# Performance work log

Hardware: AMD Instinct MI355X
Metric: run time of the kernel (lower is better)

## Reference

```python
import math
import jax, jax.numpy as jnp
import numpy as np

B, L, D, H = 8, 512, 768, 12
DK = D // H  # 64


def setup_inputs() -> dict:
    key = jax.random.key(0)
    ks = jax.random.split(key, 8)
    x = jax.random.normal(ks[0], (B, L, D), dtype=jnp.float32)
    mask = jnp.zeros((B, L), dtype=jnp.float32)            # 0 = valid, -10000 = pad (torch convention here)
    roots_label = jax.random.randint(ks[1], (B, L), 0, 2, dtype=jnp.int32)
    root_mask = jnp.ones((B, L), dtype=jnp.int32)          # only checked for not-None in the original
    W_SCALE = 0.02  # keep exp(scores) well-conditioned, as trained weights would
    Wq = jax.random.normal(ks[2], (D, D), dtype=jnp.float32) * W_SCALE
    bq = jnp.zeros((D,), dtype=jnp.float32)
    Wk = jax.random.normal(ks[3], (D, D), dtype=jnp.float32) * W_SCALE
    bk = jnp.zeros((D,), dtype=jnp.float32)
    Wr = jax.random.normal(ks[4], (D, 1), dtype=jnp.float32) * W_SCALE
    br = jnp.zeros((1,), dtype=jnp.float32)
    return {"x": x, "mask": mask, "roots_label": roots_label, "root_mask": root_mask,
            "Wq": Wq, "bq": bq, "Wk": Wk, "bk": bk, "Wr": Wr, "br": br}


def _matrix_tree_multi(scores, root):
    # scores: [B,H,L,L], root: [B,L,1]  (multi-head branch of _getMatrixTree_multi)
    A = jnp.exp(scores)                                   # [B,H,L,L]
    R = jnp.broadcast_to(jnp.exp(root)[..., 0][:, None, :], A.shape[:3])  # [B,H,L]
    col_sum = jnp.sum(A, axis=2)                          # [B,H,L]  (torch.sum(A, 2))
    eye = jnp.eye(A.shape[-1], dtype=A.dtype)
    # LL = diag(col_sum) - A + diag(R)
    LL = (col_sum + R)[..., :, None] * eye - A * (1.0 - eye) - A * eye + A * eye  # keep exact: diag(col_sum+R) - A
    LL = (col_sum + R)[..., :, None] * eye - A
    LL_inv = jnp.linalg.inv(LL)                           # [B,H,L,L]
    LL_inv_diag = jnp.diagonal(LL_inv, axis1=-2, axis2=-1)  # [B,H,L]
    d0 = R * LL_inv_diag                                  # root marginals [B,H,L]
    tmp1 = A * LL_inv_diag[..., None, :]                  # = transpose(A^T * diag[...,:,None])
    tmp2 = A * jnp.swapaxes(LL_inv, -2, -1)
    d = tmp1 - tmp2                                       # edge marginals [B,H,L,L]
    return d, d0


def reference(x, mask, roots_label, root_mask, Wq, bq, Wk, bk, Wr, br):
    key = x @ Wk + bk                                     # [B,L,D]
    query = (x @ Wq + bq) / math.sqrt(D)
    root = x @ Wr + br                                    # [B,L,1]
    q = query.reshape(B, L, H, DK).transpose(0, 2, 1, 3)  # [B,H,L,DK]
    k = key.reshape(B, L, H, DK).transpose(0, 2, 1, 3)
    scores = jnp.einsum('bhqd,bhkd->bhqk', q, k)          # [B,H,L,L]
    m = mask / -10000.0                                   # 1 at padded positions
    root = jnp.clip(root - m[:, :, None] * 50.0, -40.0, None)
    sm = jnp.broadcast_to(m[:, None, :, None], (B, H, L, L))  # scores_mask
    scores = jnp.clip(scores - sm * 50.0 - jnp.swapaxes(sm, -2, -1) * 50.0, -40.0, None)
    d, d0 = _matrix_tree_multi(scores, root)
    # root BCE loss summed over heads, masked-mean with labels
    labels = roots_label.reshape(-1).astype(jnp.float32)  # [B*L]
    p = jnp.clip(d0.astype(jnp.float32), 1e-5, 1.0 - 1e-5)
    p_h = jnp.moveaxis(p, 1, 0).reshape(H, -1)            # [H, B*L]
    bce = -(labels * jnp.log(p_h) + (1.0 - labels) * jnp.log(1.0 - p_h))
    loss_root = (bce.sum(axis=0) * labels).mean()
    attn = jnp.swapaxes(d, -2, -1)
    sm_sym = (sm + jnp.swapaxes(sm, -2, -1)).astype(bool)
    attn = jnp.where(sm_sym, 0.0, attn)
    context = jnp.einsum('bhqk,bkd->bhqd', attn, x)       # [B,H,L,D]
    return context, d, d0, loss_root
```

## Files before the change

kernel.cpp:

```cpp
#include <hip/hip_runtime.h>
#include <hip/hip_bf16.h>
#include <math.h>


#define INV_SQRT_D 0.03608439182435161f

typedef short bf16x8 __attribute__((ext_vector_type(8)));
typedef float f32x4 __attribute__((ext_vector_type(4)));
typedef unsigned int u32x4 __attribute__((ext_vector_type(4)));

__device__ __forceinline__ void mm_micro(const float* At, const float* Bt,
                                         float acc[8][8], int tx, int ty)
{
#pragma unroll
  for (int t = 0; t < 16; ++t) {
    const float4 a0 = *(const float4*)(At + t*132 + ty*8);
    const float4 a1 = *(const float4*)(At + t*132 + ty*8 + 4);
    const float4 b0 = *(const float4*)(Bt + t*132 + tx*8);
    const float4 b1 = *(const float4*)(Bt + t*132 + tx*8 + 4);
    const float a[8] = {a0.x,a0.y,a0.z,a0.w,a1.x,a1.y,a1.z,a1.w};
    const float b[8] = {b0.x,b0.y,b0.z,b0.w,b1.x,b1.y,b1.z,b1.w};
#pragma unroll
    for (int i = 0; i < 8; ++i)
#pragma unroll
      for (int j = 0; j < 8; ++j)
        acc[i][j] = fmaf(a[i], b[j], acc[i][j]);
  }
}

__global__ __launch_bounds__(256) void proj_kernel(
    const float* __restrict__ x,
    const float* __restrict__ Wq, const float* __restrict__ bq,
    const float* __restrict__ Wk, const float* __restrict__ bk,
    float* __restrict__ Q, float* __restrict__ Kc)
{
  const float* W; const float* bias; float* out; float scale;
  if (blockIdx.z == 0) { W = Wq; bias = bq; out = Q;  scale = INV_SQRT_D; }
  else                 { W = Wk; bias = bk; out = Kc; scale = 1.0f; }

  __shared__ __align__(16) float At[16*132];
  __shared__ __align__(16) float Bt[16*132];

  const int tx = threadIdx.x, ty = threadIdx.y;
  const int tid = ty*16 + tx;
  const int row0 = blockIdx.y * 128, col0 = blockIdx.x * 128;
  const int lt = tid & 15, lr = tid >> 4;
  const int bc = tid & 127, btr = tid >> 7;

  float acc[8][8] = {};

  for (int kk = 0; kk < 768; kk += 16) {
#pragma unroll
    for (int u = 0; u < 8; ++u) {
      const int r = lr + 16*u;
      At[lt*132 + r] = x[(size_t)(row0 + r)*768 + kk + lt];
    }
#pragma unroll
    for (int u = 0; u < 8; ++u) {
      const int t = btr + 2*u;
      Bt[t*132 + bc] = W[(size_t)(kk + t)*768 + col0 + bc];
    }
    __syncthreads();
    mm_micro(At, Bt, acc, tx, ty);
    __syncthreads();
  }

#pragma unroll
  for (int i = 0; i < 8; ++i) {
    const int r = row0 + ty*8 + i;
#pragma unroll
    for (int j = 0; j < 8; j += 4) {
      const int c = col0 + tx*8 + j;
      float4 v;
      v.x = (acc[i][j+0] + bias[c+0]) * scale;
      v.y = (acc[i][j+1] + bias[c+1]) * scale;
      v.z = (acc[i][j+2] + bias[c+2]) * scale;
      v.w = (acc[i][j+3] + bias[c+3]) * scale;
      *(float4*)(out + (size_t)r*768 + c) = v;
    }
  }
}

__global__ __launch_bounds__(256) void root_kernel(
    const float* __restrict__ x, const float* __restrict__ Wr,
    const float* __restrict__ br, const float* __restrict__ mask,
    float* __restrict__ Rv, float* __restrict__ mv)
{
  const int n = blockIdx.x*4 + (threadIdx.x >> 6);
  const int lane = threadIdx.x & 63;
  float s = 0.0f;
  for (int c = lane; c < 768; c += 64) s += x[(size_t)n*768 + c] * Wr[c];
#pragma unroll
  for (int off = 32; off > 0; off >>= 1) s += __shfl_down(s, off, 64);
  if (lane == 0) {
    const float root = s + br[0];
    const float m = mask[n] * (-1e-4f);
    Rv[n] = expf(fmaxf(root - m*50.0f, -40.0f));
    mv[n] = m;
  }
}

__global__ __launch_bounds__(256) void scores_kernel(
    const float* __restrict__ Qs, const float* __restrict__ Ks,
    const float* __restrict__ mv, float* __restrict__ A)
{
  const int bh = blockIdx.z, b = bh / 12, h = bh % 12;
  const int i0 = blockIdx.y * 128, j0 = blockIdx.x * 128;
  __shared__ __align__(16) float At[16*132];
  __shared__ __align__(16) float Bt[16*132];
  const int tx = threadIdx.x, ty = threadIdx.y;
  const int tid = ty*16 + tx;
  const int lt = tid & 15, lr = tid >> 4;
  const size_t qbase = (size_t)(b*512 + i0)*768 + h*64;
  const size_t kbase = (size_t)(b*512 + j0)*768 + h*64;

  float acc[8][8] = {};

  for (int kk = 0; kk < 64; kk += 16) {
#pragma unroll
    for (int u = 0; u < 8; ++u) {
      const int r = lr + 16*u;
      At[lt*132 + r] = Qs[qbase + (size_t)r*768 + kk + lt];
      Bt[lt*132 + r] = Ks[kbase + (size_t)r*768 + kk + lt];
    }
    __syncthreads();
    mm_micro(At, Bt, acc, tx, ty);
    __syncthreads();
  }

  float mi[8], mj[8];
#pragma unroll
  for (int i = 0; i < 8; ++i) mi[i] = mv[b*512 + i0 + ty*8 + i];
#pragma unroll
  for (int j = 0; j < 8; ++j) mj[j] = mv[b*512 + j0 + tx*8 + j];

#pragma unroll
  for (int i = 0; i < 8; ++i) {
    const size_t rowb = (size_t)(bh*512 + i0 + ty*8 + i)*512;
#pragma unroll
    for (int j = 0; j < 8; j += 4) {
      float4 v;
      v.x = expf(fmaxf(acc[i][j+0] - (mi[i]+mj[j+0])*50.0f, -40.0f));
      v.y = expf(fmaxf(acc[i][j+1] - (mi[i]+mj[j+1])*50.0f, -40.0f));
      v.z = expf(fmaxf(acc[i][j+2] - (mi[i]+mj[j+2])*50.0f, -40.0f));
      v.w = expf(fmaxf(acc[i][j+3] - (mi[i]+mj[j+3])*50.0f, -40.0f));
      *(float4*)(A + rowb + j0 + tx*8 + j) = v;
    }
  }
}

__global__ __launch_bounds__(256) void pack_x_kernel(
    const float* __restrict__ x, unsigned int* __restrict__ xh,
    unsigned int* __restrict__ xl)
{
  const int gid = blockIdx.x*256 + threadIdx.x;
  const int k2g = gid / 192;
  const int cc  = (gid - k2g*192) * 4;
  const unsigned int* xb = (const unsigned int*)x;
  const size_t s0 = (size_t)(2*k2g)*768 + cc;
  const uint4 r0 = *(const uint4*)(xb + s0);
  const uint4 r1 = *(const uint4*)(xb + s0 + 768);
  unsigned int hw[4], lw[4];
#pragma unroll
  for (int i = 0; i < 4; ++i) {
    const unsigned int u0 = ((const unsigned int*)&r0)[i];
    const unsigned int u1 = ((const unsigned int*)&r1)[i];
    const unsigned int h0 = (u0 + 0x7FFFu + ((u0 >> 16) & 1u)) >> 16;
    const unsigned int h1 = (u1 + 0x7FFFu + ((u1 >> 16) & 1u)) >> 16;
    hw[i] = h0 | (h1 << 16);
    const float rs0 = __uint_as_float(u0) - __uint_as_float(h0 << 16);
    const float rs1 = __uint_as_float(u1) - __uint_as_float(h1 << 16);
    lw[i] = __builtin_amdgcn_perm(__float_as_uint(rs1), __float_as_uint(rs0),
                                  0x07060302u);
  }
  const size_t o = (size_t)k2g*768 + cc;
  *(uint4*)(xh + o) = make_uint4(hw[0], hw[1], hw[2], hw[3]);
  *(uint4*)(xl + o) = make_uint4(lw[0], lw[1], lw[2], lw[3]);
}

__global__ void colsum_kernel(const float* __restrict__ A, float* __restrict__ colsum)
{
  const int bh = blockIdx.y;
  const int j = blockIdx.x*256 + threadIdx.x;
  const float* Ab = A + (size_t)bh*262144;
  float s = 0.0f;
  for (int i = 0; i < 512; ++i) s += Ab[(size_t)i*512 + j];
  colsum[bh*512 + j] = s;
}

__global__ void buildM_kernel(const float* __restrict__ A, const float* __restrict__ colsum,
                              const float* __restrict__ Rv, float* __restrict__ M)
{
  const size_t g = ((size_t)blockIdx.x*256 + threadIdx.x)*4;
  const int bh = (int)(g >> 18);
  const int i = (int)((g >> 9) & 511);
  const int j = (int)(g & 511);
  const float4 a = *(const float4*)(A + g);
  float4 v; v.x = -a.x; v.y = -a.y; v.z = -a.z; v.w = -a.w;
  if (i >= j && i < j+4) {
    const float dadd = colsum[bh*512 + i] + Rv[(bh/12)*512 + i];
    ((float*)&v)[i - j] += dadd;
  }
  *(float4*)(M + g) = v;
}

__global__ __launch_bounds__(256) void gj_inv_kernel(
    const float* __restrict__ M, float* __restrict__ Mp,
    float* __restrict__ Inv, int k0)
{
  const float* const Mg  = M   + (size_t)blockIdx.x * 262144;
  float* const Mpg       = Mp  + (size_t)blockIdx.x * 32768;
  float* const Ig        = Inv + (size_t)blockIdx.x * 4096;
  const int tid = threadIdx.x;

  if (tid >= 64) {
    const int t = tid - 64;
    for (int p = 0; p < 43; ++p) {
      const int idx = p*192 + t;
      if (idx < 8192) {
        const int r = idx >> 7, c = (idx & 127) * 4;
        *(float4*)(Mpg + (size_t)r*512 + c) =
            *(const float4*)(Mg + (size_t)(k0 + r)*512 + c);
      }
    }
    return;
  }

  const int lane = tid;
  float w[64];
  {
    const float* src = Mg + (size_t)(k0 + lane)*512 + k0;
#pragma unroll
    for (int q = 0; q < 16; ++q) {
      const float4 t4 = *(const float4*)(src + q*4);
      w[q*4+0]=t4.x; w[q*4+1]=t4.y; w[q*4+2]=t4.z; w[q*4+3]=t4.w;
    }
  }

  float fcur = w[0];
#pragma unroll 1
  for (int kk = 0; kk < 64; ++kk) {
    float rj[64];
#pragma unroll
    for (int j = 0; j < 64; ++j) rj[j] = __shfl(w[j], kk);
    const float pv = __shfl(fcur, kk);
    const float p  = 1.0f / pv;
    const bool isp = (lane == kk);
    const float alpha = isp ? p : -fcur * p;
    float fnext = fcur;
#pragma unroll
    for (int j = 0; j < 64; ++j) {
      const float base = isp ? 0.0f : w[j];
      float val = fmaf(alpha, rj[j], base);
      if (j == kk) val = alpha;
      w[j] = val;
      if (j == kk + 1) fnext = val;
    }
    fcur = fnext;
  }

  {
    float* dst = Ig + lane*64;
#pragma unroll
    for (int q = 0; q < 16; ++q)
      *(float4*)(dst + q*4) = make_float4(w[q*4+0], w[q*4+1], w[q*4+2], w[q*4+3]);
  }
}

__global__ __launch_bounds__(256) void gj_w_kernel(
    float* __restrict__ M, const float* __restrict__ Inv, int k0)
{
  const int bh = blockIdx.y;
  const int row0 = blockIdx.x * 128;
  float* const Mg = M + (size_t)bh*262144;
  const float* const Ig = Inv + (size_t)bh*4096;

  __shared__ __align__(16) float Ct[16*132];
  __shared__ __align__(16) float It[16*68];

  const int tx = threadIdx.x, ty = threadIdx.y;
  const int tid = ty*16 + tx;
  const int lt = tid & 15, lr = tid >> 4;

  float acc[8][4] = {};

  for (int kc = 0; kc < 64; kc += 16) {
#pragma unroll
    for (int u = 0; u < 8; ++u) {
      const int r = lr + 16*u;
      Ct[lt*132 + r] = Mg[(size_t)(row0 + r)*512 + k0 + kc + lt];
    }
    {
      const int j = tid & 63, t0 = tid >> 6;
#pragma unroll
      for (int u = 0; u < 4; ++u) {
        const int t = t0*4 + u;
        It[t*68 + j] = Ig[(kc + t)*64 + j];
      }
    }
    __syncthreads();
#pragma unroll
    for (int t = 0; t < 16; ++t) {
      const float4 a0 = *(const float4*)(Ct + t*132 + ty*8);
      const float4 a1 = *(const float4*)(Ct + t*132 + ty*8 + 4);
      const float4 b  = *(const float4*)(It + t*68 + tx*4);
      const float a[8] = {a0.x,a0.y,a0.z,a0.w,a1.x,a1.y,a1.z,a1.w};
      const float bb[4] = {b.x,b.y,b.z,b.w};
#pragma unroll
      for (int i = 0; i < 8; ++i)
#pragma unroll
        for (int j = 0; j < 4; ++j)
          acc[i][j] = fmaf(a[i], bb[j], acc[i][j]);
    }
    __syncthreads();
  }

#pragma unroll
  for (int i = 0; i < 8; ++i) {
    const int irow = row0 + ty*8 + i;
    float4 v;
    if (irow >= k0 && irow < k0 + 64) {
      v = *(const float4*)(Ig + (irow - k0)*64 + tx*4);
    } else {
      v = make_float4(-acc[i][0], -acc[i][1], -acc[i][2], -acc[i][3]);
    }
    *(float4*)(Mg + (size_t)irow*512 + k0 + tx*4) = v;
  }
}

__global__ __launch_bounds__(256) void gj_update_kernel(
    float* __restrict__ M, const float* __restrict__ Mp, int k0)
{
  const int bh = blockIdx.z;
  const int row0 = blockIdx.y * 128, col0 = blockIdx.x * 128;
  float* const Mg = M + (size_t)bh*262144;
  const float* const Mpg = Mp + (size_t)bh*32768;

  __shared__ __align__(16) float At[16*132];
  __shared__ __align__(16) float Bt[16*132];
  const int tx = threadIdx.x, ty = threadIdx.y;
  const int tid = ty*16 + tx;
  const int lt = tid & 15, lr = tid >> 4;
  const int bc = tid & 127, btr = tid >> 7;

  float acc[8][8] = {};

  for (int kc = 0; kc < 64; kc += 16) {
#pragma unroll
    for (int u = 0; u < 8; ++u) {
      const int r = lr + 16*u;
      At[lt*132 + r] = Mg[(size_t)(row0 + r)*512 + k0 + kc + lt];
    }
#pragma unroll
    for (int u = 0; u < 8; ++u) {
      const int t = btr + 2*u;
      Bt[t*132 + bc] = Mpg[(size_t)(kc + t)*512 + col0 + bc];
    }
    __syncthreads();
    mm_micro(At, Bt, acc, tx, ty);
    __syncthreads();
  }

#pragma unroll
  for (int ii = 0; ii < 8; ++ii) {
    const int irow = row0 + ty*8 + ii;
    const bool inP = (irow >= k0) && (irow < k0 + 64);
#pragma unroll
    for (int jj = 0; jj < 8; jj += 4) {
      const int jcol = col0 + tx*8 + jj;
      if (jcol >= k0 && jcol < k0 + 64) continue;
      float* cell = Mg + (size_t)irow*512 + jcol;
      float4 v = make_float4(acc[ii][jj+0], acc[ii][jj+1], acc[ii][jj+2], acc[ii][jj+3]);
      if (!inP) {
        const float4 o = *(const float4*)cell;
        v.x += o.x; v.y += o.y; v.z += o.z; v.w += o.w;
      }
      *(float4*)cell = v;
    }
  }
}

__global__ void diag_d0_kernel(const float* __restrict__ Minv, const float* __restrict__ Rv,
                               float* __restrict__ diagv, float* __restrict__ d0)
{
  const int bh = blockIdx.x, l = threadIdx.x;
  const float dg = Minv[(size_t)bh*262144 + (size_t)l*513];
  diagv[bh*512 + l] = dg;
  d0[bh*512 + l] = Rv[(bh/12)*512 + l] * dg;
}

__global__ __launch_bounds__(1024) void loss_kernel(const float* __restrict__ d0,
                                                    const int* __restrict__ labels,
                                                    float* __restrict__ loss)
{
  float acc = 0.0f;
  for (int n = threadIdx.x; n < 4096; n += 1024) {
    if (labels[n] != 0) {
      const int b = n >> 9, l = n & 511;
      float s = 0.0f;
#pragma unroll
      for (int h = 0; h < 12; ++h) {
        float p = d0[(size_t)(b*12 + h)*512 + l];
        p = fminf(fmaxf(p, 1e-5f), 1.0f - 1e-5f);
        s -= logf(p);
      }
      acc += s;
    }
  }
  __shared__ float red[16];
#pragma unroll
  for (int off = 32; off > 0; off >>= 1) acc += __shfl_down(acc, off, 64);
  const int wv = threadIdx.x >> 6, ln = threadIdx.x & 63;
  if (ln == 0) red[wv] = acc;
  __syncthreads();
  if (threadIdx.x == 0) {
    float t = 0.0f;
    for (int w2 = 0; w2 < 16; ++w2) t += red[w2];
    loss[0] = t * (1.0f/4096.0f);
  }
}

__global__ __launch_bounds__(256) void finalize_d_kernel(
    float* __restrict__ dmat, const float* __restrict__ Minv, const float* __restrict__ diagv)
{
  const int bh = blockIdx.z;
  const int i0 = blockIdx.y*64, j0 = blockIdx.x*64;
  __shared__ float t[64][65];
  const int tx = threadIdx.x, ty = threadIdx.y;
  const size_t mbase = (size_t)bh*262144;
  for (int jj = ty; jj < 64; jj += 4)
    t[jj][tx] = Minv[mbase + (size_t)(j0+jj)*512 + i0 + tx];
  __syncthreads();
  const float dg_j = diagv[bh*512 + j0 + tx];
  for (int ii = ty; ii < 64; ii += 4) {
    const size_t idx = mbase + (size_t)(i0+ii)*512 + j0 + tx;
    dmat[idx] = dmat[idx] * (dg_j - t[tx][ii]);
  }
}

__global__ __launch_bounds__(256) void context_packed_kernel(
    const float* __restrict__ dmat, const unsigned int* __restrict__ xh,
    const unsigned int* __restrict__ xl, const float* __restrict__ mv,
    float* __restrict__ ctx)
{
  const int bh = blockIdx.z + 8, b = bh / 12;
  const int q0 = blockIdx.y << 7;
  const int c0 = blockIdx.x << 7;

  __shared__ __align__(16) unsigned int AhL[16*132];
  __shared__ __align__(16) unsigned int AlL[16*132];
  __shared__ __align__(16) unsigned int BhL[16*132];
  __shared__ __align__(16) unsigned int BlL[16*132];

  const int tid = threadIdx.x;
  const int w = tid >> 6, l = tid & 63;
  const int wq = w >> 1, wc = w & 1;
  const int l15 = l & 15, g = l >> 4;
  const int q4 = tid & 31, pp = tid >> 5;

  const size_t dbase = (size_t)bh*262144;
  const int xrow0 = b*256;

  float mq[4];
  {
    const float4 t4 = *(const float4*)(mv + b*512 + q0 + q4*4);
    mq[0]=t4.x; mq[1]=t4.y; mq[2]=t4.z; mq[3]=t4.w;
  }

  f32x4 acc[4][4] = {};

  for (int kk = 0; kk < 512; kk += 32) {
    __syncthreads();
#pragma unroll
    for (int s = 0; s < 2; ++s) {
      const int k2 = pp + 8*s;
      const int krow = kk + 2*k2;
      const float mk0 = mv[b*512 + krow];
      const float mk1 = mv[b*512 + krow + 1];
      const uint4 r0 = *(const uint4*)(dmat + dbase + (size_t)krow*512 + q0 + q4*4);
      const uint4 r1 = *(const uint4*)(dmat + dbase + (size_t)(krow+1)*512 + q0 + q4*4);
      unsigned int hw[4], lw[4];
#pragma unroll
      for (int i = 0; i < 4; ++i) {
        unsigned int v0 = ((const unsigned int*)&r0)[i];
        unsigned int v1 = ((const unsigned int*)&r1)[i];
        v0 = ((mk0 + mq[i]) != 0.0f) ? 0u : v0;
        v1 = ((mk1 + mq[i]) != 0.0f) ? 0u : v1;
        hw[i] = __builtin_amdgcn_perm(v1, v0, 0x07060302u);
        const float f0 = __uint_as_float(v0) - __uint_as_float(v0 & 0xffff0000u);
        const float f1 = __uint_as_float(v1) - __uint_as_float(v1 & 0xffff0000u);
        lw[i] = __builtin_amdgcn_perm(__float_as_uint(f1), __float_as_uint(f0),
                                      0x07060302u);
      }
      *(uint4*)(AhL + k2*132 + q4*4) = make_uint4(hw[0], hw[1], hw[2], hw[3]);
      *(uint4*)(AlL + k2*132 + q4*4) = make_uint4(lw[0], lw[1], lw[2], lw[3]);
      const size_t xi = (size_t)(xrow0 + (kk >> 1) + k2)*768 + c0 + q4*4;
      *(uint4*)(BhL + k2*132 + q4*4) = *(const uint4*)(xh + xi);
      *(uint4*)(BlL + k2*132 + q4*4) = *(const uint4*)(xl + xi);
    }
    __syncthreads();

    u32x4 ah[4], al[4], bhv[4], blv[4];
#pragma unroll
    for (int mi = 0; mi < 4; ++mi) {
      const int col = wq*64 + mi*16 + l15;
#pragma unroll
      for (int d2 = 0; d2 < 4; ++d2) {
        ah[mi][d2] = AhL[(4*g + d2)*132 + col];
        al[mi][d2] = AlL[(4*g + d2)*132 + col];
      }
    }
#pragma unroll
    for (int ni = 0; ni < 4; ++ni) {
      const int col = wc*64 + ni*16 + l15;
#pragma unroll
      for (int d2 = 0; d2 < 4; ++d2) {
        bhv[ni][d2] = BhL[(4*g + d2)*132 + col];
        blv[ni][d2] = BlL[(4*g + d2)*132 + col];
      }
    }

#pragma unroll
    for (int mi = 0; mi < 4; ++mi) {
      const bf16x8 Ah = __builtin_bit_cast(bf16x8, ah[mi]);
      const bf16x8 Al = __builtin_bit_cast(bf16x8, al[mi]);
#pragma unroll
      for (int ni = 0; ni < 4; ++ni) {
        const bf16x8 Bh = __builtin_bit_cast(bf16x8, bhv[ni]);
        const bf16x8 Bl = __builtin_bit_cast(bf16x8, blv[ni]);
        acc[mi][ni] = __builtin_amdgcn_mfma_f32_16x16x32_bf16(Ah, Bh, acc[mi][ni], 0, 0, 0);
        acc[mi][ni] = __builtin_amdgcn_mfma_f32_16x16x32_bf16(Ah, Bl, acc[mi][ni], 0, 0, 0);
        acc[mi][ni] = __builtin_amdgcn_mfma_f32_16x16x32_bf16(Al, Bh, acc[mi][ni], 0, 0, 0);
      }
    }
  }

#pragma unroll
  for (int mi = 0; mi < 4; ++mi) {
    const int row = q0 + wq*64 + mi*16 + g*4;
#pragma unroll
    for (int ni = 0; ni < 4; ++ni) {
      const int col = c0 + wc*64 + ni*16 + l15;
#pragma unroll
      for (int r = 0; r < 4; ++r)
        ctx[((size_t)bh*512 + row + r)*768 + col] = acc[mi][ni][r];
    }
  }
}

__device__ __forceinline__ unsigned int pack_bf16x2(float v)
{
  const unsigned int u = __float_as_uint(v);
  const unsigned int hi = (u + 0x7FFFu + ((u >> 16) & 1u)) >> 16;
  const float hf = __uint_as_float(hi << 16);
  const unsigned int lo = __float_as_uint(v - hf) >> 16;
  return hi | (lo << 16);
}

__global__ __launch_bounds__(256) void context_mfma_kernel(
    const float* __restrict__ dmat, const float* __restrict__ x,
    const float* __restrict__ mv, float* __restrict__ ctx)
{
  const int bh = blockIdx.z, b = bh / 12;
  const int q0 = blockIdx.y << 7;
  const int c0 = blockIdx.x << 7;

  __shared__ unsigned int As[32*133];
  __shared__ unsigned int Bs[32*133];

  const int tid = threadIdx.x;
  const int w = tid >> 6, l = tid & 63;
  const int wq = w >> 1, wc = w & 1;
  const int l15 = l & 15, g = l >> 4;
  const int q4 = tid & 31, kr0 = tid >> 5;

  const size_t dbase = (size_t)bh*262144;
  const size_t xbase = (size_t)b*393216;

  float mq[4];
  {
    const float4 t4 = *(const float4*)(mv + b*512 + q0 + q4*4);
    mq[0]=t4.x; mq[1]=t4.y; mq[2]=t4.z; mq[3]=t4.w;
  }

  f32x4 acc[4][4] = {};

  for (int kk = 0; kk < 512; kk += 32) {
    __syncthreads();
#pragma unroll
    for (int p = 0; p < 4; ++p) {
      const int kr = kr0 + 8*p;
      const int krow = kk + kr;
      const float mk = mv[b*512 + krow];
      const float4 av = *(const float4*)(dmat + dbase + (size_t)krow*512 + q0 + q4*4);
      const float4 bv = *(const float4*)(x + xbase + (size_t)krow*768 + c0 + q4*4);
      unsigned int* aw = As + kr*133 + q4*4;
      unsigned int* bw = Bs + kr*133 + q4*4;
      aw[0] = pack_bf16x2(((mk + mq[0]) != 0.0f) ? 0.0f : av.x);
      aw[1] = pack_bf16x2(((mk + mq[1]) != 0.0f) ? 0.0f : av.y);
      aw[2] = pack_bf16x2(((mk + mq[2]) != 0.0f) ? 0.0f : av.z);
      aw[3] = pack_bf16x2(((mk + mq[3]) != 0.0f) ? 0.0f : av.w);
      bw[0] = pack_bf16x2(bv.x);
      bw[1] = pack_bf16x2(bv.y);
      bw[2] = pack_bf16x2(bv.z);
      bw[3] = pack_bf16x2(bv.w);
    }
    __syncthreads();

    u32x4 ah[4], al[4], bhv[4], blv[4];
#pragma unroll
    for (int mi = 0; mi < 4; ++mi) {
      const unsigned int* base = As + g*8*133 + (wq*64 + mi*16 + l15);
      unsigned int u[8];
#pragma unroll
      for (int e = 0; e < 8; ++e) u[e] = base[e*133];
#pragma unroll
      for (int d2 = 0; d2 < 4; ++d2) {
        ah[mi][d2] = __builtin_amdgcn_perm(u[2*d2+1], u[2*d2], 0x05040100u);
        al[mi][d2] = __builtin_amdgcn_perm(u[2*d2+1], u[2*d2], 0x07060302u);
      }
    }
#pragma unroll
    for (int ni = 0; ni < 4; ++ni) {
      const unsigned int* base = Bs + g*8*133 + (wc*64 + ni*16 + l15);
      unsigned int u[8];
#pragma unroll
      for (int e = 0; e < 8; ++e) u[e] = base[e*133];
#pragma unroll
      for (int d2 = 0; d2 < 4; ++d2) {
        bhv[ni][d2] = __builtin_amdgcn_perm(u[2*d2+1], u[2*d2], 0x05040100u);
        blv[ni][d2] = __builtin_amdgcn_perm(u[2*d2+1], u[2*d2], 0x07060302u);
      }
    }

#pragma unroll
    for (int mi = 0; mi < 4; ++mi) {
      const bf16x8 Ah = __builtin_bit_cast(bf16x8, ah[mi]);
      const bf16x8 Al = __builtin_bit_cast(bf16x8, al[mi]);
#pragma unroll
      for (int ni = 0; ni < 4; ++ni) {
        const bf16x8 Bh = __builtin_bit_cast(bf16x8, bhv[ni]);
        const bf16x8 Bl = __builtin_bit_cast(bf16x8, blv[ni]);
        acc[mi][ni] = __builtin_amdgcn_mfma_f32_16x16x32_bf16(Ah, Bh, acc[mi][ni], 0, 0, 0);
        acc[mi][ni] = __builtin_amdgcn_mfma_f32_16x16x32_bf16(Ah, Bl, acc[mi][ni], 0, 0, 0);
        acc[mi][ni] = __builtin_amdgcn_mfma_f32_16x16x32_bf16(Al, Bh, acc[mi][ni], 0, 0, 0);
      }
    }
  }

#pragma unroll
  for (int mi = 0; mi < 4; ++mi) {
    const int row = q0 + wq*64 + mi*16 + g*4;
#pragma unroll
    for (int ni = 0; ni < 4; ++ni) {
      const int col = c0 + wc*64 + ni*16 + l15;
#pragma unroll
      for (int r = 0; r < 4; ++r)
        ctx[((size_t)bh*512 + row + r)*768 + col] = acc[mi][ni][r];
    }
  }
}

extern "C" void kernel_launch(void* const* d_in, const int* in_sizes, int n_in,
                              void* d_out, int out_size, void* d_ws, size_t ws_size,
                              hipStream_t stream)
{
  (void)in_sizes; (void)n_in; (void)out_size; (void)ws_size;

  const float* x    = (const float*)d_in[0];
  const float* mask = (const float*)d_in[1];
  const int*   roots= (const int*)d_in[2];
  const float* Wq   = (const float*)d_in[4];
  const float* bq   = (const float*)d_in[5];
  const float* Wk   = (const float*)d_in[6];
  const float* bk   = (const float*)d_in[7];
  const float* Wr   = (const float*)d_in[8];
  const float* br   = (const float*)d_in[9];

  float* out        = (float*)d_out;
  float* ctx_region = out;
  float* d_region   = out + 37748736;
  float* d0_region  = out + 62914560;
  float* loss_ptr   = out + 62963712;

  float* Qs = ctx_region;
  float* Ks = ctx_region + 3145728;
  float* Mv = ctx_region + 6291456;
  float* Mp = ctx_region + 31457280;
  float* Invs = ctx_region + 34603008;

  unsigned int* xh = (unsigned int*)ctx_region;
  unsigned int* xl = (unsigned int*)ctx_region + 1572864;

  float* ws     = (float*)d_ws;
  float* Rv     = ws;
  float* mv     = ws + 4096;
  float* colsum = ws + 8192;
  float* diagv  = ws + 57344;

  proj_kernel   <<<dim3(6,32,2),  dim3(16,16), 0, stream>>>(x, Wq, bq, Wk, bk, Qs, Ks);
  root_kernel   <<<dim3(1024),    dim3(256),   0, stream>>>(x, Wr, br, mask, Rv, mv);
  scores_kernel <<<dim3(4,4,96),  dim3(16,16), 0, stream>>>(Qs, Ks, mv, d_region);
  pack_x_kernel <<<dim3(1536),    dim3(256),   0, stream>>>(x, xh, xl);
  colsum_kernel <<<dim3(2,96),    dim3(256),   0, stream>>>(d_region, colsum);
  buildM_kernel <<<dim3(24576),   dim3(256),   0, stream>>>(d_region, colsum, Rv, Mv);

  for (int step = 0; step < 8; ++step) {
    const int k0 = step * 64;
    gj_inv_kernel   <<<dim3(96),     dim3(256),   0, stream>>>(Mv, Mp, Invs, k0);
    gj_w_kernel     <<<dim3(4,96),   dim3(16,16), 0, stream>>>(Mv, Invs, k0);
    gj_update_kernel<<<dim3(4,4,96), dim3(16,16), 0, stream>>>(Mv, Mp, k0);
  }

  diag_d0_kernel<<<dim3(96),      dim3(512),   0, stream>>>(Mv, Rv, diagv, d0_region);
  loss_kernel   <<<dim3(1),       dim3(1024),  0, stream>>>(d0_region, roots, loss_ptr);
  finalize_d_kernel<<<dim3(8,8,96), dim3(64,4), 0, stream>>>(d_region, Mv, diagv);
  context_packed_kernel<<<dim3(6,4,88), dim3(256), 0, stream>>>(d_region, xh, xl, mv, ctx_region);
  context_mfma_kernel  <<<dim3(6,4,8),  dim3(256), 0, stream>>>(d_region, x, mv, ctx_region);
}
```

Measured before the change: 1.909 ms.

## Use split-bf16 MFMA for Q/K projection and move panel copy into gj_w

Replaces the FP32 SIMT projection GEMM with a bf16 MFMA kernel using a three-term hi/lo split to keep near-FP32 accuracy, with weights pre-split by a new pack kernel. Also moves the pivot-row panel copy out of the single-block-per-head inversion kernel into the wider gj_w kernel, shrinking gj_inv to one wave. This removes FP32 FMA cost in the projection and the serial panel copy from each elimination step. The cost is an extra packing pass, more workspace, and a possible race if panel rows are modified before other blocks copy them.

```diff
diff --git a/kernel.cpp b/kernel.cpp
--- a/kernel.cpp
+++ b/kernel.cpp
@@ -28,138 +28,23 @@
   }
 }
 
-__global__ __launch_bounds__(256) void proj_kernel(
-    const float* __restrict__ x,
-    const float* __restrict__ Wq, const float* __restrict__ bq,
-    const float* __restrict__ Wk, const float* __restrict__ bk,
-    float* __restrict__ Q, float* __restrict__ Kc)
-{
-  const float* W; const float* bias; float* out; float scale;
-  if (blockIdx.z == 0) { W = Wq; bias = bq; out = Q;  scale = INV_SQRT_D; }
-  else                 { W = Wk; bias = bk; out = Kc; scale = 1.0f; }
-
-  __shared__ __align__(16) float At[16*132];
-  __shared__ __align__(16) float Bt[16*132];
-
-  const int tx = threadIdx.x, ty = threadIdx.y;
-  const int tid = ty*16 + tx;
-  const int row0 = blockIdx.y * 128, col0 = blockIdx.x * 128;
-  const int lt = tid & 15, lr = tid >> 4;
-  const int bc = tid & 127, btr = tid >> 7;
-
-  float acc[8][8] = {};
-
-  for (int kk = 0; kk < 768; kk += 16) {
-#pragma unroll
-    for (int u = 0; u < 8; ++u) {
-      const int r = lr + 16*u;
-      At[lt*132 + r] = x[(size_t)(row0 + r)*768 + kk + lt];
-    }
-#pragma unroll
-    for (int u = 0; u < 8; ++u) {
-      const int t = btr + 2*u;
-      Bt[t*132 + bc] = W[(size_t)(kk + t)*768 + col0 + bc];
-    }
-    __syncthreads();
-    mm_micro(At, Bt, acc, tx, ty);
-    __syncthreads();
-  }
-
-#pragma unroll
-  for (int i = 0; i < 8; ++i) {
-    const int r = row0 + ty*8 + i;
-#pragma unroll
-    for (int j = 0; j < 8; j += 4) {
-      const int c = col0 + tx*8 + j;
-      float4 v;
-      v.x = (acc[i][j+0] + bias[c+0]) * scale;
-      v.y = (acc[i][j+1] + bias[c+1]) * scale;
-      v.z = (acc[i][j+2] + bias[c+2]) * scale;
-      v.w = (acc[i][j+3] + bias[c+3]) * scale;
-      *(float4*)(out + (size_t)r*768 + c) = v;
-    }
-  }
-}
-
-__global__ __launch_bounds__(256) void root_kernel(
-    const float* __restrict__ x, const float* __restrict__ Wr,
-    const float* __restrict__ br, const float* __restrict__ mask,
-    float* __restrict__ Rv, float* __restrict__ mv)
-{
-  const int n = blockIdx.x*4 + (threadIdx.x >> 6);
-  const int lane = threadIdx.x & 63;
-  float s = 0.0f;
-  for (int c = lane; c < 768; c += 64) s += x[(size_t)n*768 + c] * Wr[c];
-#pragma unroll
-  for (int off = 32; off > 0; off >>= 1) s += __shfl_down(s, off, 64);
-  if (lane == 0) {
-    const float root = s + br[0];
-    const float m = mask[n] * (-1e-4f);
-    Rv[n] = expf(fmaxf(root - m*50.0f, -40.0f));
-    mv[n] = m;
-  }
-}
-
-__global__ __launch_bounds__(256) void scores_kernel(
-    const float* __restrict__ Qs, const float* __restrict__ Ks,
-    const float* __restrict__ mv, float* __restrict__ A)
-{
-  const int bh = blockIdx.z, b = bh / 12, h = bh % 12;
-  const int i0 = blockIdx.y * 128, j0 = blockIdx.x * 128;
-  __shared__ __align__(16) float At[16*132];
-  __shared__ __align__(16) float Bt[16*132];
-  const int tx = threadIdx.x, ty = threadIdx.y;
-  const int tid = ty*16 + tx;
-  const int lt = tid & 15, lr = tid >> 4;
-  const size_t qbase = (size_t)(b*512 + i0)*768 + h*64;
-  const size_t kbase = (size_t)(b*512 + j0)*768 + h*64;
-
-  float acc[8][8] = {};
-
-  for (int kk = 0; kk < 64; kk += 16) {
-#pragma unroll
-    for (int u = 0; u < 8; ++u) {
-      const int r = lr + 16*u;
-      At[lt*132 + r] = Qs[qbase + (size_t)r*768 + kk + lt];
-      Bt[lt*132 + r] = Ks[kbase + (size_t)r*768 + kk + lt];
-    }
-    __syncthreads();
-    mm_micro(At, Bt, acc, tx, ty);
-    __syncthreads();
-  }
-
-  float mi[8], mj[8];
-#pragma unroll
-  for (int i = 0; i < 8; ++i) mi[i] = mv[b*512 + i0 + ty*8 + i];
-#pragma unroll
-  for (int j = 0; j < 8; ++j) mj[j] = mv[b*512 + j0 + tx*8 + j];
-
-#pragma unroll
-  for (int i = 0; i < 8; ++i) {
-    const size_t rowb = (size_t)(bh*512 + i0 + ty*8 + i)*512;
-#pragma unroll
-    for (int j = 0; j < 8; j += 4) {
-      float4 v;
-      v.x = expf(fmaxf(acc[i][j+0] - (mi[i]+mj[j+0])*50.0f, -40.0f));
-      v.y = expf(fmaxf(acc[i][j+1] - (mi[i]+mj[j+1])*50.0f, -40.0f));
-      v.z = expf(fmaxf(acc[i][j+2] - (mi[i]+mj[j+2])*50.0f, -40.0f));
-      v.w = expf(fmaxf(acc[i][j+3] - (mi[i]+mj[j+3])*50.0f, -40.0f));
-      *(float4*)(A + rowb + j0 + tx*8 + j) = v;
-    }
-  }
-}
-
-__global__ __launch_bounds__(256) void pack_x_kernel(
-    const float* __restrict__ x, unsigned int* __restrict__ xh,
-    unsigned int* __restrict__ xl)
+__global__ __launch_bounds__(256) void pack_w_kernel(
+    const float* __restrict__ Wq, const float* __restrict__ Wk,
+    unsigned int* __restrict__ Wqh, unsigned int* __restrict__ Wql,
+    unsigned int* __restrict__ Wkh, unsigned int* __restrict__ Wkl)
 {
   const int gid = blockIdx.x*256 + threadIdx.x;
-  const int k2g = gid / 192;
-  const int cc  = (gid - k2g*192) * 4;
-  const unsigned int* xb = (const unsigned int*)x;
-  const size_t s0 = (size_t)(2*k2g)*768 + cc;
-  const uint4 r0 = *(const uint4*)(xb + s0);
-  const uint4 r1 = *(const uint4*)(xb + s0 + 768);
+  const int m = gid >= 73728;
+  const int id = m ? gid - 73728 : gid;
+  const int k2 = id / 192;
+  const int cc = (id - k2*192) * 4;
+  const float* W = m ? Wk : Wq;
+  unsigned int* Oh = m ? Wkh : Wqh;
+  unsigned int* Ol = m ? Wkl : Wql;
+  const unsigned int* wb = (const unsigned int*)W;
+  const size_t s0 = (size_t)(2*k2)*768 + cc;
+  const uint4 r0 = *(const uint4*)(wb + s0);
+  const uint4 r1 = *(const uint4*)(wb + s0 + 768);
   unsigned int hw[4], lw[4];
 #pragma unroll
   for (int i = 0; i < 4; ++i) {
@@ -173,6 +58,214 @@
     lw[i] = __builtin_amdgcn_perm(__float_as_uint(rs1), __float_as_uint(rs0),
                                   0x07060302u);
   }
+  const size_t o = (size_t)k2*768 + cc;
+  *(uint4*)(Oh + o) = make_uint4(hw[0], hw[1], hw[2], hw[3]);
+  *(uint4*)(Ol + o) = make_uint4(lw[0], lw[1], lw[2], lw[3]);
+}
+
+__global__ __launch_bounds__(256) void proj_mfma_kernel(
+    const float* __restrict__ x,
+    const unsigned int* __restrict__ Wqh, const unsigned int* __restrict__ Wql,
+    const unsigned int* __restrict__ Wkh, const unsigned int* __restrict__ Wkl,
+    const float* __restrict__ bq, const float* __restrict__ bk,
+    float* __restrict__ Q, float* __restrict__ Kc)
+{
+  const unsigned int* Wh; const unsigned int* Wl;
+  const float* bias; float* out; float scale;
+  if (blockIdx.z == 0) { Wh = Wqh; Wl = Wql; bias = bq; out = Q;  scale = INV_SQRT_D; }
+  else                 { Wh = Wkh; Wl = Wkl; bias = bk; out = Kc; scale = 1.0f; }
+
+  const int row0 = blockIdx.y << 7;
+  const int col0 = blockIdx.x << 7;
+
+  __shared__ __align__(16) unsigned int AhL[16*132];
+  __shared__ __align__(16) unsigned int AlL[16*132];
+  __shared__ __align__(16) unsigned int BhL[16*132];
+  __shared__ __align__(16) unsigned int BlL[16*132];
+
+  const int tid = threadIdx.x;
+  const int w = tid >> 6, l = tid & 63;
+  const int wq = w >> 1, wc = w & 1;
+  const int l15 = l & 15, g = l >> 4;
+  const int q4 = tid & 31, pp = tid >> 5;
+  const int an = tid & 127, ahh = tid >> 7;
+
+  f32x4 acc[4][4] = {};
+
+  for (int kk = 0; kk < 768; kk += 32) {
+    __syncthreads();
+#pragma unroll
+    for (int s = 0; s < 2; ++s) {
+      const int k2 = pp + 8*s;
+      const size_t wi = (size_t)((kk >> 1) + k2)*768 + col0 + q4*4;
+      *(uint4*)(BhL + k2*132 + q4*4) = *(const uint4*)(Wh + wi);
+      *(uint4*)(BlL + k2*132 + q4*4) = *(const uint4*)(Wl + wi);
+    }
+    {
+      const float* xr = x + (size_t)(row0 + an)*768 + kk + ahh*16;
+      const uint4 v0 = *(const uint4*)(xr + 0);
+      const uint4 v1 = *(const uint4*)(xr + 4);
+      const uint4 v2 = *(const uint4*)(xr + 8);
+      const uint4 v3 = *(const uint4*)(xr + 12);
+      const unsigned int uu[16] = {v0.x,v0.y,v0.z,v0.w, v1.x,v1.y,v1.z,v1.w,
+                                   v2.x,v2.y,v2.z,v2.w, v3.x,v3.y,v3.z,v3.w};
+#pragma unroll
+      for (int pr = 0; pr < 8; ++pr) {
+        const unsigned int a0 = uu[2*pr], a1 = uu[2*pr+1];
+        const unsigned int hw = __builtin_amdgcn_perm(a1, a0, 0x07060302u);
+        const float f0 = __uint_as_float(a0) - __uint_as_float(a0 & 0xffff0000u);
+        const float f1 = __uint_as_float(a1) - __uint_as_float(a1 & 0xffff0000u);
+        const unsigned int lw = __builtin_amdgcn_perm(__float_as_uint(f1),
+                                                      __float_as_uint(f0),
+                                                      0x07060302u);
+        const int k2 = ahh*8 + pr;
+        AhL[k2*132 + an] = hw;
+        AlL[k2*132 + an] = lw;
+      }
+    }
+    __syncthreads();
+
+    u32x4 ah[4], al[4], bhv[4], blv[4];
+#pragma unroll
+    for (int mi = 0; mi < 4; ++mi) {
+      const int col = wq*64 + mi*16 + l15;
+#pragma unroll
+      for (int d2 = 0; d2 < 4; ++d2) {
+        ah[mi][d2] = AhL[(4*g + d2)*132 + col];
+        al[mi][d2] = AlL[(4*g + d2)*132 + col];
+      }
+    }
+#pragma unroll
+    for (int ni = 0; ni < 4; ++ni) {
+      const int col = wc*64 + ni*16 + l15;
+#pragma unroll
+      for (int d2 = 0; d2 < 4; ++d2) {
+        bhv[ni][d2] = BhL[(4*g + d2)*132 + col];
+        blv[ni][d2] = BlL[(4*g + d2)*132 + col];
+      }
+    }
+
+#pragma unroll
+    for (int mi = 0; mi < 4; ++mi) {
+      const bf16x8 Ah = __builtin_bit_cast(bf16x8, ah[mi]);
+      const bf16x8 Al = __builtin_bit_cast(bf16x8, al[mi]);
+#pragma unroll
+      for (int ni = 0; ni < 4; ++ni) {
+        const bf16x8 Bh = __builtin_bit_cast(bf16x8, bhv[ni]);
+        const bf16x8 Bl = __builtin_bit_cast(bf16x8, blv[ni]);
+        acc[mi][ni] = __builtin_amdgcn_mfma_f32_16x16x32_bf16(Ah, Bh, acc[mi][ni], 0, 0, 0);
+        acc[mi][ni] = __builtin_amdgcn_mfma_f32_16x16x32_bf16(Ah, Bl, acc[mi][ni], 0, 0, 0);
+        acc[mi][ni] = __builtin_amdgcn_mfma_f32_16x16x32_bf16(Al, Bh, acc[mi][ni], 0, 0, 0);
+      }
+    }
+  }
+
+#pragma unroll
+  for (int mi = 0; mi < 4; ++mi) {
+    const int row = row0 + wq*64 + mi*16 + g*4;
+#pragma unroll
+    for (int ni = 0; ni < 4; ++ni) {
+      const int col = col0 + wc*64 + ni*16 + l15;
+      const float bs = bias[col];
+#pragma unroll
+      for (int r = 0; r < 4; ++r)
+        out[(size_t)(row + r)*768 + col] = (acc[mi][ni][r] + bs) * scale;
+    }
+  }
+}
+
+__global__ __launch_bounds__(256) void root_kernel(
+    const float* __restrict__ x, const float* __restrict__ Wr,
+    const float* __restrict__ br, const float* __restrict__ mask,
+    float* __restrict__ Rv, float* __restrict__ mv)
+{
+  const int n = blockIdx.x*4 + (threadIdx.x >> 6);
+  const int lane = threadIdx.x & 63;
+  float s = 0.0f;
+  for (int c = lane; c < 768; c += 64) s += x[(size_t)n*768 + c] * Wr[c];
+#pragma unroll
+  for (int off = 32; off > 0; off >>= 1) s += __shfl_down(s, off, 64);
+  if (lane == 0) {
+    const float root = s + br[0];
+    const float m = mask[n] * (-1e-4f);
+    Rv[n] = expf(fmaxf(root - m*50.0f, -40.0f));
+    mv[n] = m;
+  }
+}
+
+__global__ __launch_bounds__(256) void scores_kernel(
+    const float* __restrict__ Qs, const float* __restrict__ Ks,
+    const float* __restrict__ mv, float* __restrict__ A)
+{
+  const int bh = blockIdx.z, b = bh / 12, h = bh % 12;
+  const int i0 = blockIdx.y * 128, j0 = blockIdx.x * 128;
+  __shared__ __align__(16) float At[16*132];
+  __shared__ __align__(16) float Bt[16*132];
+  const int tx = threadIdx.x, ty = threadIdx.y;
+  const int tid = ty*16 + tx;
+  const int lt = tid & 15, lr = tid >> 4;
+  const size_t qbase = (size_t)(b*512 + i0)*768 + h*64;
+  const size_t kbase = (size_t)(b*512 + j0)*768 + h*64;
+
+  float acc[8][8] = {};
+
+  for (int kk = 0; kk < 64; kk += 16) {
+#pragma unroll
+    for (int u = 0; u < 8; ++u) {
+      const int r = lr + 16*u;
+      At[lt*132 + r] = Qs[qbase + (size_t)r*768 + kk + lt];
+      Bt[lt*132 + r] = Ks[kbase + (size_t)r*768 + kk + lt];
+    }
+    __syncthreads();
+    mm_micro(At, Bt, acc, tx, ty);
+    __syncthreads();
+  }
+
+  float mi[8], mj[8];
+#pragma unroll
+  for (int i = 0; i < 8; ++i) mi[i] = mv[b*512 + i0 + ty*8 + i];
+#pragma unroll
+  for (int j = 0; j < 8; ++j) mj[j] = mv[b*512 + j0 + tx*8 + j];
+
+#pragma unroll
+  for (int i = 0; i < 8; ++i) {
+    const size_t rowb = (size_t)(bh*512 + i0 + ty*8 + i)*512;
+#pragma unroll
+    for (int j = 0; j < 8; j += 4) {
+      float4 v;
+      v.x = expf(fmaxf(acc[i][j+0] - (mi[i]+mj[j+0])*50.0f, -40.0f));
+      v.y = expf(fmaxf(acc[i][j+1] - (mi[i]+mj[j+1])*50.0f, -40.0f));
+      v.z = expf(fmaxf(acc[i][j+2] - (mi[i]+mj[j+2])*50.0f, -40.0f));
+      v.w = expf(fmaxf(acc[i][j+3] - (mi[i]+mj[j+3])*50.0f, -40.0f));
+      *(float4*)(A + rowb + j0 + tx*8 + j) = v;
+    }
+  }
+}
+
+__global__ __launch_bounds__(256) void pack_x_kernel(
+    const float* __restrict__ x, unsigned int* __restrict__ xh,
+    unsigned int* __restrict__ xl)
+{
+  const int gid = blockIdx.x*256 + threadIdx.x;
+  const int k2g = gid / 192;
+  const int cc  = (gid - k2g*192) * 4;
+  const unsigned int* xb = (const unsigned int*)x;
+  const size_t s0 = (size_t)(2*k2g)*768 + cc;
+  const uint4 r0 = *(const uint4*)(xb + s0);
+  const uint4 r1 = *(const uint4*)(xb + s0 + 768);
+  unsigned int hw[4], lw[4];
+#pragma unroll
+  for (int i = 0; i < 4; ++i) {
+    const unsigned int u0 = ((const unsigned int*)&r0)[i];
+    const unsigned int u1 = ((const unsigned int*)&r1)[i];
+    const unsigned int h0 = (u0 + 0x7FFFu + ((u0 >> 16) & 1u)) >> 16;
+    const unsigned int h1 = (u1 + 0x7FFFu + ((u1 >> 16) & 1u)) >> 16;
+    hw[i] = h0 | (h1 << 16);
+    const float rs0 = __uint_as_float(u0) - __uint_as_float(h0 << 16);
+    const float rs1 = __uint_as_float(u1) - __uint_as_float(h1 << 16);
+    lw[i] = __builtin_amdgcn_perm(__float_as_uint(rs1), __float_as_uint(rs0),
+                                  0x07060302u);
+  }
   const size_t o = (size_t)k2g*768 + cc;
   *(uint4*)(xh + o) = make_uint4(hw[0], hw[1], hw[2], hw[3]);
   *(uint4*)(xl + o) = make_uint4(lw[0], lw[1], lw[2], lw[3]);
@@ -204,29 +297,13 @@
   *(float4*)(M + g) = v;
 }
 
-__global__ __launch_bounds__(256) void gj_inv_kernel(
-    const float* __restrict__ M, float* __restrict__ Mp,
-    float* __restrict__ Inv, int k0)
-{
-  const float* const Mg  = M   + (size_t)blockIdx.x * 262144;
-  float* const Mpg       = Mp  + (size_t)blockIdx.x * 32768;
-  float* const Ig        = Inv + (size_t)blockIdx.x * 4096;
-  const int tid = threadIdx.x;
-
-  if (tid >= 64) {
-    const int t = tid - 64;
-    for (int p = 0; p < 43; ++p) {
-      const int idx = p*192 + t;
-      if (idx < 8192) {
-        const int r = idx >> 7, c = (idx & 127) * 4;
-        *(float4*)(Mpg + (size_t)r*512 + c) =
-            *(const float4*)(Mg + (size_t)(k0 + r)*512 + c);
-      }
-    }
-    return;
-  }
-
-  const int lane = tid;
+__global__ __launch_bounds__(64) void gj_inv_kernel(
+    const float* __restrict__ M, float* __restrict__ Inv, int k0)
+{
+  const float* const Mg = M + (size_t)blockIdx.x * 262144;
+  float* const Ig = Inv + (size_t)blockIdx.x * 4096;
+  const int lane = threadIdx.x;
+
   float w[64];
   {
     const float* src = Mg + (size_t)(k0 + lane)*512 + k0;
@@ -268,11 +345,13 @@
 }
 
 __global__ __launch_bounds__(256) void gj_w_kernel(
-    float* __restrict__ M, const float* __restrict__ Inv, int k0)
+    float* __restrict__ M, float* __restrict__ Mp,
+    const float* __restrict__ Inv, int k0)
 {
   const int bh = blockIdx.y;
   const int row0 = blockIdx.x * 128;
   float* const Mg = M + (size_t)bh*262144;
+  float* const Mpg = Mp + (size_t)bh*32768;
   const float* const Ig = Inv + (size_t)bh*4096;
 
   __shared__ __align__(16) float Ct[16*132];
@@ -281,6 +360,18 @@
   const int tx = threadIdx.x, ty = threadIdx.y;
   const int tid = ty*16 + tx;
   const int lt = tid & 15, lr = tid >> 4;
+
+  {
+    const int rq = blockIdx.x;
+    const int c4 = (tid & 127) * 4;
+    const int rr = tid >> 7;
+#pragma unroll
+    for (int u = 0; u < 8; ++u) {
+      const int r = rq*16 + u*2 + rr;
+      *(float4*)(Mpg + (size_t)r*512 + c4) =
+          *(const float4*)(Mg + (size_t)(k0 + r)*512 + c4);
+    }
+  }
 
   float acc[8][4] = {};
 
@@ -692,13 +783,19 @@
   unsigned int* xh = (unsigned int*)ctx_region;
   unsigned int* xl = (unsigned int*)ctx_region + 1572864;
 
+  unsigned int* Wqh = (unsigned int*)ctx_region + 34996224;
+  unsigned int* Wql = Wqh + 294912;
+  unsigned int* Wkh = Wql + 294912;
+  unsigned int* Wkl = Wkh + 294912;
+
   float* ws     = (float*)d_ws;
   float* Rv     = ws;
   float* mv     = ws + 4096;
   float* colsum = ws + 8192;
   float* diagv  = ws + 57344;
 
-  proj_kernel   <<<dim3(6,32,2),  dim3(16,16), 0, stream>>>(x, Wq, bq, Wk, bk, Qs, Ks);
+  pack_w_kernel <<<dim3(576),     dim3(256),   0, stream>>>(Wq, Wk, Wqh, Wql, Wkh, Wkl);
+  proj_mfma_kernel<<<dim3(6,32,2), dim3(256),  0, stream>>>(x, Wqh, Wql, Wkh, Wkl, bq, bk, Qs, Ks);
   root_kernel   <<<dim3(1024),    dim3(256),   0, stream>>>(x, Wr, br, mask, Rv, mv);
   scores_kernel <<<dim3(4,4,96),  dim3(16,16), 0, stream>>>(Qs, Ks, mv, d_region);
   pack_x_kernel <<<dim3(1536),    dim3(256),   0, stream>>>(x, xh, xl);
@@ -707,8 +804,8 @@
 
   for (int step = 0; step < 8; ++step) {
     const int k0 = step * 64;
-    gj_inv_kernel   <<<dim3(96),     dim3(256),   0, stream>>>(Mv, Mp, Invs, k0);
-    gj_w_kernel     <<<dim3(4,96),   dim3(16,16), 0, stream>>>(Mv, Invs, k0);
+    gj_inv_kernel   <<<dim3(96),     dim3(64),    0, stream>>>(Mv, Invs, k0);
+    gj_w_kernel     <<<dim3(4,96),   dim3(16,16), 0, stream>>>(Mv, Mp, Invs, k0);
     gj_update_kernel<<<dim3(4,4,96), dim3(16,16), 0, stream>>>(Mv, Mp, k0);
   }
 
```

Measured after the change: 1.863 ms. 1.02x faster.
